# Optimization experiments

Hardware: AMD Instinct MI355X
Metric: run time of the kernel (lower is better)

## Reference

```python
import jax, jax.numpy as jnp
import numpy as np

MAX_CHILD = 64  # max trie branching factor (padding width for per-row child windows)


def setup_inputs() -> dict:
    key = jax.random.key(0)
    B, D, V, N = 1024, 1024, 32000, 200000
    k1, k2, k3, k4 = jax.random.split(key, 4)
    x = jax.random.normal(k1, (B, D), dtype=jnp.float32)
    weight = jax.random.normal(k2, (V, D), dtype=jnp.float32) * 0.02
    bias = jax.random.normal(k3, (V,), dtype=jnp.float32) * 0.02
    # Build a consistent CompactCSRTrie: offsets [N+1], tokens/child_nodes [E]
    rng = np.random.default_rng(0)
    deg = rng.integers(1, MAX_CHILD + 1, size=N)
    offsets = np.zeros(N + 1, dtype=np.int32)
    offsets[1:] = np.cumsum(deg)
    E = int(offsets[-1])
    tokens = rng.integers(0, V, size=E).astype(np.int32)
    child_nodes = rng.integers(0, N, size=E).astype(np.int32)
    cur_node = jax.random.randint(k4, (B,), 0, N, dtype=jnp.int32)
    return {
        "x": x,
        "weight": weight,
        "bias": bias,
        "cur_node": cur_node,
        "offsets": jnp.asarray(offsets),
        "tokens": jnp.asarray(tokens),
        "child_nodes": jnp.asarray(child_nodes),
        "step": 1,
    }


def reference(x, weight, bias, cur_node, offsets, tokens, child_nodes, step):
    # Dense GEMM part of the fused kernel: logits = x @ W^T + b  -> [B, V]
    logits = jnp.einsum("bd,vd->bv", x, weight) + bias
    B, V = logits.shape

    # CSR trie traversal: per row, the children of cur_node are
    # tokens[offsets[cur]:offsets[cur+1]] (valid next tokens) and
    # child_nodes[...] (next trie nodes). Gather a padded MAX_CHILD window.
    start = offsets[cur_node]                              # [B]
    deg = offsets[cur_node + 1] - start                    # [B]
    pos = jnp.arange(MAX_CHILD, dtype=start.dtype)         # [C]
    idx = jnp.minimum(start[:, None] + pos[None, :], tokens.shape[0] - 1)  # [B, C]
    valid = pos[None, :] < deg[:, None]                    # [B, C] bool

    tok = tokens[idx]                                      # [B, C] valid token columns
    child = child_nodes[idx]                               # [B, C] next trie nodes

    # Validity masking: only valid child tokens keep their logit, rest -> -inf
    rows = jnp.arange(B)[:, None]
    mask = jnp.zeros((B, V), dtype=bool).at[rows, tok].max(valid)
    masked_logits = jnp.where(mask, logits, -jnp.inf)

    next_nodes = jnp.where(valid, child, -1)               # [B, C], -1 padded
    valid_idxs = jnp.where(valid, tok, -1)                 # [B, C], -1 padded
    return next_nodes, valid_idxs, masked_logits
```

## Files before the change

### kernel.cpp

```cpp
#include <hip/hip_runtime.h>
#include <math.h>

#define B_ 1024
#define D_ 1024
#define V_ 32000
#define MAXC 64
#define NSLICE 16
#define SLICE_TOK 2000
#define SLICE_F4 500

#define NEG_FILL (-3.0e38f)

typedef float vfloat4 __attribute__((ext_vector_type(4)));

__global__ __launch_bounds__(256, 8) void constrained_linear_kernel(
    const float* __restrict__ x,
    const float* __restrict__ weight,
    const float* __restrict__ bias,
    const int* __restrict__ cur_node,
    const int* __restrict__ offsets,
    const int* __restrict__ tokens,
    const int* __restrict__ child_nodes,
    float* __restrict__ next_nodes,
    float* __restrict__ valid_idxs,
    float* __restrict__ masked_logits)
{
    __shared__ int   ltok[MAXC];
    __shared__ float lval[MAXC];

    const int bid  = blockIdx.x;
    const int b    = bid >> 4;
    const int q    = bid & (NSLICE - 1);
    const int tid  = threadIdx.x;
    const int wave = tid >> 6;
    const int lane = tid & 63;

    const int cur = cur_node[b];
    const int start = offsets[cur];
    int deg = offsets[cur + 1] - start;
    if (deg > MAXC) deg = MAXC;

    int tok = -1;
    bool match = false;
    float bv = 0.0f;
    const int slot = wave * 16 + (lane & 15);
    if (lane < 16 && slot < deg) {
        tok = tokens[start + slot];
        match = ((unsigned)tok / SLICE_TOK) == (unsigned)q;
    }
    if (lane < 16) ltok[wave * 16 + lane] = match ? tok : -1;
    if (match) bv = bias[tok];
    unsigned long long mask = __ballot(match);

    if (tid < 4) {
        const int c = q * 4 + tid;
        float nn = -1.0f, vi = -1.0f;
        if (c < deg) {
            const int e = start + c;
            nn = (float)child_nodes[e];
            vi = (float)tokens[e];
        }
        next_nodes[b * MAXC + c] = nn;
        valid_idxs[b * MAXC + c] = vi;
    }

    float* ml_row = masked_logits + (size_t)b * V_;
    vfloat4* ml4 = reinterpret_cast<vfloat4*>(ml_row);
    const vfloat4 sent = {NEG_FILL, NEG_FILL, NEG_FILL, NEG_FILL};
    for (int i = q * SLICE_F4 + tid; i < (q + 1) * SLICE_F4; i += 256)
        __builtin_nontemporal_store(sent, &ml4[i]);

    const float4* x4 = reinterpret_cast<const float4*>(x + (size_t)b * D_);
    while (mask) {
        const int s = __builtin_ctzll(mask);
        mask &= mask - 1;
        const int t = __shfl(tok, s);
        const float4* w4 = reinterpret_cast<const float4*>(weight + (size_t)t * D_);
        float acc = 0.0f;
        #pragma unroll
        for (int k = 0; k < 4; ++k) {
            const float4 wv = w4[k * 64 + lane];
            const float4 xv = x4[k * 64 + lane];
            acc += wv.x * xv.x + wv.y * xv.y + wv.z * xv.z + wv.w * xv.w;
        }
        #pragma unroll
        for (int off = 32; off > 0; off >>= 1)
            acc += __shfl_xor(acc, off);
        if (lane == s)
            lval[wave * 16 + s] = acc + bv;
    }

    __syncthreads();

    if (tid < MAXC) {
        const int t = ltok[tid];
        if (t >= 0)
            ml_row[t] = lval[tid];
    }
}

extern "C" void kernel_launch(void* const* d_in, const int* in_sizes, int n_in,
                              void* d_out, int out_size, void* d_ws, size_t ws_size,
                              hipStream_t stream) {
    const float* x           = (const float*)d_in[0];
    const float* weight      = (const float*)d_in[1];
    const float* bias        = (const float*)d_in[2];
    const int*   cur_node    = (const int*)d_in[3];
    const int*   offsets     = (const int*)d_in[4];
    const int*   tokens      = (const int*)d_in[5];
    const int*   child_nodes = (const int*)d_in[6];

    float* out = (float*)d_out;
    float* next_nodes    = out;
    float* valid_idxs    = out + (size_t)B_ * MAXC;
    float* masked_logits = out + 2 * (size_t)B_ * MAXC;

    constrained_linear_kernel<<<B_ * NSLICE, 256, 0, stream>>>(
        x, weight, bias, cur_node, offsets, tokens, child_nodes,
        next_nodes, valid_idxs, masked_logits);
}
```

Baseline: 48.28 us.

## Split each row into two vocab halves with round-robin dot-product assignment across waves

```diff
diff --git a/kernel.cpp b/kernel.cpp
--- a/kernel.cpp
+++ b/kernel.cpp
@@ -5,9 +5,8 @@
 #define D_ 1024
 #define V_ 32000
 #define MAXC 64
-#define NSLICE 16
-#define SLICE_TOK 2000
-#define SLICE_F4 500
+#define HALF_TOK 16000
+#define HALF_F4  4000
 
 #define NEG_FILL (-3.0e38f)
 
@@ -29,8 +28,8 @@
     __shared__ float lval[MAXC];
 
     const int bid  = blockIdx.x;
-    const int b    = bid >> 4;
-    const int q    = bid & (NSLICE - 1);
+    const int b    = bid >> 1;
+    const int h    = bid & 1;
     const int tid  = threadIdx.x;
     const int wave = tid >> 6;
     const int lane = tid & 63;
@@ -43,17 +42,40 @@
     int tok = -1;
     bool match = false;
     float bv = 0.0f;
-    const int slot = wave * 16 + (lane & 15);
-    if (lane < 16 && slot < deg) {
-        tok = tokens[start + slot];
-        match = ((unsigned)tok / SLICE_TOK) == (unsigned)q;
+    if (lane < deg) {
+        tok = tokens[start + lane];
+        match = ((unsigned)tok / HALF_TOK) == (unsigned)h;
     }
-    if (lane < 16) ltok[wave * 16 + lane] = match ? tok : -1;
     if (match) bv = bias[tok];
-    unsigned long long mask = __ballot(match);
+    if (wave == 0) ltok[lane] = match ? tok : -1;
+    const unsigned long long mask = __ballot(match);
 
-    if (tid < 4) {
-        const int c = q * 4 + tid;
+    unsigned long long mym = 0;
+    {
+        unsigned long long m = mask;
+        int ord = 0;
+        while (m) {
+            const unsigned long long bit = m & (~m + 1);
+            m &= m - 1;
+            if ((ord & 3) == wave) mym |= bit;
+            ++ord;
+        }
+    }
+
+    float4 wA[4];
+    int sA = -1, tA = 0;
+    if (mym) {
+        sA = __builtin_ctzll(mym);
+        mym &= mym - 1;
+        tA = __shfl(tok, sA);
+        const float4* w4 = reinterpret_cast<const float4*>(weight + (size_t)tA * D_);
+        #pragma unroll
+        for (int k = 0; k < 4; ++k)
+            wA[k] = w4[k * 64 + lane];
+    }
+
+    if (tid < 32) {
+        const int c = h * 32 + tid;
         float nn = -1.0f, vi = -1.0f;
         if (c < deg) {
             const int e = start + c;
@@ -67,13 +89,25 @@
     float* ml_row = masked_logits + (size_t)b * V_;
     vfloat4* ml4 = reinterpret_cast<vfloat4*>(ml_row);
     const vfloat4 sent = {NEG_FILL, NEG_FILL, NEG_FILL, NEG_FILL};
-    for (int i = q * SLICE_F4 + tid; i < (q + 1) * SLICE_F4; i += 256)
+    for (int i = h * HALF_F4 + tid; i < (h + 1) * HALF_F4; i += 256)
         __builtin_nontemporal_store(sent, &ml4[i]);
 
     const float4* x4 = reinterpret_cast<const float4*>(x + (size_t)b * D_);
-    while (mask) {
-        const int s = __builtin_ctzll(mask);
-        mask &= mask - 1;
+    if (sA >= 0) {
+        float acc = 0.0f;
+        #pragma unroll
+        for (int k = 0; k < 4; ++k) {
+            const float4 xv = x4[k * 64 + lane];
+            acc += wA[k].x * xv.x + wA[k].y * xv.y + wA[k].z * xv.z + wA[k].w * xv.w;
+        }
+        #pragma unroll
+        for (int off = 32; off > 0; off >>= 1)
+            acc += __shfl_xor(acc, off);
+        if (lane == sA) lval[sA] = acc + bv;
+    }
+    while (mym) {
+        const int s = __builtin_ctzll(mym);
+        mym &= mym - 1;
         const int t = __shfl(tok, s);
         const float4* w4 = reinterpret_cast<const float4*>(weight + (size_t)t * D_);
         float acc = 0.0f;
@@ -86,8 +120,7 @@
         #pragma unroll
         for (int off = 32; off > 0; off >>= 1)
             acc += __shfl_xor(acc, off);
-        if (lane == s)
-            lval[wave * 16 + s] = acc + bv;
+        if (lane == s) lval[s] = acc + bv;
     }
 
     __syncthreads();
@@ -115,7 +148,7 @@
     float* valid_idxs    = out + (size_t)B_ * MAXC;
     float* masked_logits = out + 2 * (size_t)B_ * MAXC;
 
-    constrained_linear_kernel<<<B_ * NSLICE, 256, 0, stream>>>(
+    constrained_linear_kernel<<<B_ * 2, 256, 0, stream>>>(
         x, weight, bias, cur_node, offsets, tokens, child_nodes,
         next_nodes, valid_idxs, masked_logits);
 }
```

New measurement: 50.58 us. 1.05x slower.
